# Optimization experiments

Measured on AMD Instinct MI355X. Metric: run time of the kernel, lower is better.

Reference implementation:

```python
import jax, jax.numpy as jnp
import numpy as np

HIDDEN = 4096
N_HEADS = 32
N_KV_HEADS = 8
HEAD_DIM = HIDDEN // N_HEADS  # 128
N_GROUPS = N_HEADS // N_KV_HEADS  # 4
ROPE_THETA = 10000.0
NEG_INF = -1e9


def fake_quant(x):
    """Symmetric per-tensor int8 fake quantization (quantize -> dequantize)."""
    scale = jnp.maximum(jnp.max(jnp.abs(x)) / 127.0, 1e-8)
    return jnp.clip(jnp.round(x / scale), -127.0, 127.0) * scale


def q_linear(x, W):
    # torch Linear: y = x @ W.T ; both operands fake-quantized (dequant-inline GEMM)
    return jnp.einsum('bsh,oh->bso', fake_quant(x), fake_quant(W))


def rope_cos_sin(position_ids, head_dim, dtype):
    inv_freq = 1.0 / (ROPE_THETA ** (jnp.arange(0, head_dim, 2, dtype=jnp.float32) / head_dim))
    freqs = position_ids.astype(jnp.float32)[..., None] * inv_freq  # [b, s, hd/2]
    emb = jnp.concatenate([freqs, freqs], axis=-1)                   # [b, s, hd]
    return jnp.cos(emb).astype(dtype), jnp.sin(emb).astype(dtype)


def rotate_half(x):
    x1, x2 = jnp.split(x, 2, axis=-1)
    return jnp.concatenate([-x2, x1], axis=-1)


def setup_inputs() -> dict:
    key = jax.random.key(0)
    ks = jax.random.split(key, 6)
    b, s = 2, 1024
    hidden_states = jax.random.normal(ks[0], (b, s, HIDDEN), dtype=jnp.float32)
    # additive causal mask [b, 1, q, kv]
    causal = jnp.where(jnp.tril(jnp.ones((s, s), dtype=bool)), 0.0, NEG_INF).astype(jnp.float32)
    attention_mask = jnp.broadcast_to(causal[None, None], (b, 1, s, s))
    position_ids = jnp.broadcast_to(jnp.arange(s, dtype=jnp.int64)[None, :], (b, s))
    winit = 1.0 / np.sqrt(HIDDEN)
    Wq = jax.random.normal(ks[1], (HIDDEN, HIDDEN), dtype=jnp.float32) * winit
    Wk = jax.random.normal(ks[2], (N_KV_HEADS * HEAD_DIM, HIDDEN), dtype=jnp.float32) * winit
    Wv = jax.random.normal(ks[3], (N_KV_HEADS * HEAD_DIM, HIDDEN), dtype=jnp.float32) * winit
    Wo = jax.random.normal(ks[4], (HIDDEN, HIDDEN), dtype=jnp.float32) * winit
    return {"hidden_states": hidden_states, "attention_mask": attention_mask,
            "position_ids": position_ids, "Wq": Wq, "Wk": Wk, "Wv": Wv, "Wo": Wo}


def reference(hidden_states, attention_mask, position_ids, Wq, Wk, Wv, Wo):
    b, s, _ = hidden_states.shape
    dtype = hidden_states.dtype

    # quantized QKV projections
    q = q_linear(hidden_states, Wq).reshape(b, s, N_HEADS, HEAD_DIM).transpose(0, 2, 1, 3)
    k = q_linear(hidden_states, Wk).reshape(b, s, N_KV_HEADS, HEAD_DIM).transpose(0, 2, 1, 3)
    v = q_linear(hidden_states, Wv).reshape(b, s, N_KV_HEADS, HEAD_DIM).transpose(0, 2, 1, 3)

    # RoPE
    cos, sin = rope_cos_sin(position_ids, HEAD_DIM, dtype)  # [b, s, hd]
    cos, sin = cos[:, None], sin[:, None]                   # broadcast over heads
    q = q * cos + rotate_half(q) * sin
    k = k * cos + rotate_half(k) * sin

    # GQA: repeat kv heads
    k = jnp.repeat(k, N_GROUPS, axis=1)  # [b, H, s, hd]
    v = jnp.repeat(v, N_GROUPS, axis=1)

    # quantized QK^T (per-tensor fake quant on both operands)
    attn = jnp.einsum('bhqd,bhkd->bhqk', fake_quant(q), fake_quant(k)) / jnp.sqrt(
        jnp.asarray(HEAD_DIM, dtype=jnp.float32)).astype(dtype)
    attn = attn + attention_mask
    attn = jax.nn.softmax(attn.astype(jnp.float32), axis=-1).astype(dtype)
    # attention_dropout = 0.0 (inference)

    # quantized AV matmul
    out = jnp.einsum('bhqk,bhkd->bhqd', fake_quant(attn), fake_quant(v))
    out = out.transpose(0, 2, 1, 3).reshape(b, s, HIDDEN)
    out = q_linear(out, Wo)
    return out
```

## Files before the change

### kernel.cpp

```cpp
#include <hip/hip_runtime.h>
#include <math.h>

#define B_ 2
#define S_ 1024
#define HID 4096
#define NH 32
#define NKV 8
#define HD 128
#define LOG2E 1.44269504088896340736f

typedef short s16x8 __attribute__((ext_vector_type(8)));
typedef float f32x4 __attribute__((ext_vector_type(4)));
typedef unsigned short u16;
typedef u16 u16x4 __attribute__((ext_vector_type(4)));

__device__ __forceinline__ f32x4 mfma16(s16x8 a, s16x8 b, f32x4 c) {
  return __builtin_amdgcn_mfma_f32_16x16x32_bf16(a, b, c, 0, 0, 0);
}
__device__ __forceinline__ u16 f2bf(float f) {
  union { float f; unsigned u; } v; v.f = f;
  return (u16)(v.u >> 16);
}
__device__ __forceinline__ float get_scale(const unsigned* sc, int slot) {
  return fmaxf(__uint_as_float(sc[slot]) / 127.0f, 1e-8f);
}
__device__ __forceinline__ void gload16(const void* g, void* l) {
  __builtin_amdgcn_global_load_lds(
      (const __attribute__((address_space(1))) unsigned*)g,
      (__attribute__((address_space(3))) unsigned*)l, 16, 0, 0);
}
__device__ __forceinline__ void atomic_absmax(unsigned* out, float m, int lane) {
  #pragma unroll
  for (int o = 32; o >= 1; o >>= 1) m = fmaxf(m, __shfl_xor(m, o));
  if (lane == 0) atomicMax(out, __float_as_uint(m));
}

#define SB_() __builtin_amdgcn_sched_barrier(0)
#define PBAR() do { SB_(); __builtin_amdgcn_s_barrier(); SB_(); } while (0)
#define VM6() do { SB_(); asm volatile("s_waitcnt vmcnt(6)" ::: "memory"); } while (0)
#define VM0() do { SB_(); asm volatile("s_waitcnt vmcnt(0)" ::: "memory"); } while (0)

__global__ void absmax5_k(const float4* __restrict__ p0, const float4* __restrict__ p1,
                          const float4* __restrict__ p2, const float4* __restrict__ p3,
                          const float4* __restrict__ p4, unsigned* __restrict__ sc) {
  int r = blockIdx.y;
  const float4* x; int n4;
  if (r == 0)      { x = p0; n4 = B_ * S_ * HID / 4; }
  else if (r == 1) { x = p1; n4 = HID * HID / 4; }
  else if (r == 2) { x = p2; n4 = NKV * HD * HID / 4; }
  else if (r == 3) { x = p3; n4 = NKV * HD * HID / 4; }
  else             { x = p4; n4 = HID * HID / 4; }
  float m = 0.f;
  int stride = gridDim.x * blockDim.x;
  for (int i = blockIdx.x * blockDim.x + threadIdx.x; i < n4; i += stride) {
    float4 v = x[i];
    m = fmaxf(m, fmaxf(fmaxf(fabsf(v.x), fabsf(v.y)), fmaxf(fabsf(v.z), fabsf(v.w))));
  }
  atomic_absmax(sc + r, m, threadIdx.x & 63);
}

__global__ void quant5_k(const float4* __restrict__ p0, const float4* __restrict__ p1,
                         const float4* __restrict__ p2, const float4* __restrict__ p3,
                         const float4* __restrict__ p4,
                         u16x4* __restrict__ y0, u16x4* __restrict__ y1,
                         u16x4* __restrict__ y2, u16x4* __restrict__ y3,
                         u16x4* __restrict__ y4, const unsigned* __restrict__ sc) {
  int r = blockIdx.y;
  const float4* x; u16x4* y; int n4;
  if (r == 0)      { x = p0; y = y0; n4 = B_ * S_ * HID / 4; }
  else if (r == 1) { x = p1; y = y1; n4 = HID * HID / 4; }
  else if (r == 2) { x = p2; y = y2; n4 = NKV * HD * HID / 4; }
  else if (r == 3) { x = p3; y = y3; n4 = NKV * HD * HID / 4; }
  else             { x = p4; y = y4; n4 = HID * HID / 4; }
  float s = get_scale(sc, r);
  int stride = gridDim.x * blockDim.x;
  for (int i = blockIdx.x * blockDim.x + threadIdx.x; i < n4; i += stride) {
    float4 v = x[i];
    u16x4 o;
    o[0] = f2bf(fminf(fmaxf(rintf(v.x / s), -127.f), 127.f));
    o[1] = f2bf(fminf(fmaxf(rintf(v.y / s), -127.f), 127.f));
    o[2] = f2bf(fminf(fmaxf(rintf(v.z / s), -127.f), 127.f));
    o[3] = f2bf(fminf(fmaxf(rintf(v.w / s), -127.f), 127.f));
    y[i] = o;
  }
}

__global__ void quant_k(const float4* __restrict__ x, u16x4* __restrict__ y, int n4,
                        const unsigned* __restrict__ sc, int slot) {
  float s = get_scale(sc, slot);
  int stride = gridDim.x * blockDim.x;
  for (int i = blockIdx.x * blockDim.x + threadIdx.x; i < n4; i += stride) {
    float4 v = x[i];
    u16x4 o;
    o[0] = f2bf(fminf(fmaxf(rintf(v.x / s), -127.f), 127.f));
    o[1] = f2bf(fminf(fmaxf(rintf(v.y / s), -127.f), 127.f));
    o[2] = f2bf(fminf(fmaxf(rintf(v.z / s), -127.f), 127.f));
    o[3] = f2bf(fminf(fmaxf(rintf(v.w / s), -127.f), 127.f));
    y[i] = o;
  }
}

__global__ void add_k(const float4* __restrict__ p0, const float4* __restrict__ p1,
                      float4* __restrict__ out, int n4) {
  int stride = gridDim.x * blockDim.x;
  for (int i = blockIdx.x * blockDim.x + threadIdx.x; i < n4; i += stride) {
    float4 a = p0[i], b = p1[i];
    out[i] = make_float4(a.x + b.x, a.y + b.y, a.z + b.z, a.w + b.w);
  }
}

__device__ __forceinline__ void rdA(const u16* slot, int wm, int lr, int lg,
                                    s16x8 af[4][2]) {
  #pragma unroll
  for (int mi = 0; mi < 4; ++mi) {
    int row = wm * 64 + mi * 16 + lr;
    const char* base = (const char*)slot + row * 128;
    int sw = (row & 7) << 4;
    #pragma unroll
    for (int ks = 0; ks < 2; ++ks)
      af[mi][ks] = *(const s16x8*)(base + ((ks * 64 + lg * 16) ^ sw));
  }
}
__device__ __forceinline__ void rdB(const u16* slot, int wn, int lr, int lg,
                                    s16x8 bf[2][2]) {
  #pragma unroll
  for (int ni = 0; ni < 2; ++ni) {
    int row = wn * 32 + ni * 16 + lr;
    const char* base = (const char*)slot + row * 128;
    int sw = (row & 7) << 4;
    #pragma unroll
    for (int ks = 0; ks < 2; ++ks)
      bf[ni][ks] = *(const s16x8*)(base + ((ks * 64 + lg * 16) ^ sw));
  }
}
template <int PM, int PN>
__device__ __forceinline__ void mfma_phase(f32x4 (&acc)[2][2][4][2],
                                           const s16x8 (&af)[4][2],
                                           const s16x8 (&bf)[2][2]) {
  __builtin_amdgcn_s_setprio(1);
  #pragma unroll
  for (int mi = 0; mi < 4; ++mi)
    #pragma unroll
    for (int ni = 0; ni < 2; ++ni)
      #pragma unroll
      for (int ks = 0; ks < 2; ++ks)
        acc[PM][PN][mi][ni] = mfma16(af[mi][ks], bf[ni][ks], acc[PM][PN][mi][ni]);
  __builtin_amdgcn_s_setprio(0);
}

__device__ void gemm256(const u16* __restrict__ A, const u16* __restrict__ Bm,
                        float* __restrict__ C, int Ncols, int m0, int n0,
                        int k0, int nkt, float scale, unsigned* omax, u16* S) {
  const int tid = threadIdx.x;
  const int wave = tid >> 6, lane = tid & 63;
  const int lr = lane & 15, lg = lane >> 4;
  const int wm = wave >> 2, wn = wave & 3;
  u16* SA00 = S;          u16* SA01 = S + 8192;
  u16* SB00 = S + 16384;  u16* SB01 = S + 24576;
  u16* SA10 = S + 32768;  u16* SA11 = S + 40960;
  u16* SB10 = S + 49152;  u16* SB11 = S + 57344;
  const int r0 = tid >> 3;
  const int ce = (((tid & 7) * 16) ^ ((r0 & 7) << 4)) >> 1;
  const u16* pa0 = A + (size_t)(m0 + r0) * HID + k0 + ce;
  const u16* pa1 = pa0 + (size_t)128 * HID;
  const u16* pb0 = Bm + (size_t)(n0 + r0) * HID + k0 + ce;
  const u16* pb1 = pb0 + (size_t)128 * HID;
  const int wdst = wave * 512;
  f32x4 acc[2][2][4][2] = {};
  s16x8 af[4][2], bf[2][2];

  auto STG = [&](const u16* p, u16* slot, int tcol) {
    const u16* g = p + tcol * 64;
    gload16(g, slot + wdst);
    gload16(g + (size_t)64 * HID, slot + 4096 + wdst);
  };

  STG(pa0, SA00, 0); STG(pb0, SB00, 0); STG(pa1, SA01, 0); STG(pb1, SB01, 0);
  STG(pa0, SA10, 1); STG(pb1, SB11, 1); STG(pa1, SA11, 1);
  VM6(); PBAR();

  #pragma unroll 1
  for (int t = 0; t < nkt; t += 2) {
    const bool g2 = t + 2 < nkt, g3 = t + 3 < nkt;
    rdA(SA00, wm, lr, lg, af); rdB(SB00, wn, lr, lg, bf);
    STG(pb0, SB10, t + 1);
    PBAR(); mfma_phase<0, 0>(acc, af, bf); PBAR();
    rdB(SB01, wn, lr, lg, bf);
    if (g2) STG(pa0, SA00, t + 2);
    PBAR(); mfma_phase<0, 1>(acc, af, bf); PBAR();
    rdA(SA01, wm, lr, lg, af);
    if (g2) STG(pb1, SB01, t + 2);
    PBAR(); mfma_phase<1, 1>(acc, af, bf); PBAR();
    rdB(SB00, wn, lr, lg, bf);
    if (g2) STG(pa1, SA01, t + 2);
    PBAR(); mfma_phase<1, 0>(acc, af, bf);
    if (g2) { VM6(); } else { VM0(); }
    PBAR();
    rdA(SA10, wm, lr, lg, af); rdB(SB10, wn, lr, lg, bf);
    if (g2) STG(pb0, SB00, t + 2);
    PBAR(); mfma_phase<0, 0>(acc, af, bf); PBAR();
    rdB(SB11, wn, lr, lg, bf);
    if (g3) STG(pa0, SA10, t + 3);
    PBAR(); mfma_phase<0, 1>(acc, af, bf); PBAR();
    rdA(SA11, wm, lr, lg, af);
    if (g3) STG(pb1, SB11, t + 3);
    PBAR(); mfma_phase<1, 1>(acc, af, bf); PBAR();
    rdB(SB10, wn, lr, lg, bf);
    if (g3) STG(pa1, SA11, t + 3);
    PBAR(); mfma_phase<1, 0>(acc, af, bf); VM6(); PBAR();
  }

  float gm = 0.f;
  #pragma unroll
  for (int mh = 0; mh < 2; ++mh)
    #pragma unroll
    for (int nh = 0; nh < 2; ++nh)
      #pragma unroll
      for (int mi = 0; mi < 4; ++mi)
        #pragma unroll
        for (int ni = 0; ni < 2; ++ni) {
          size_t rbase = (size_t)(m0 + mh * 128 + wm * 64 + mi * 16 + lg * 4);
          int cb = n0 + nh * 128 + wn * 32 + ni * 16 + lr;
          #pragma unroll
          for (int r = 0; r < 4; ++r) {
            float v = acc[mh][nh][mi][ni][r] * scale;
            gm = fmaxf(gm, fabsf(v));
            C[(rbase + r) * (size_t)Ncols + cb] = v;
          }
        }
  if (omax) atomic_absmax(omax, gm, lane);
}

__global__ __launch_bounds__(512, 1) void gemm_qkv8(
    const u16* __restrict__ Xq, const u16* __restrict__ Wqb,
    const u16* __restrict__ Wkb, const u16* __restrict__ Wvb,
    float* __restrict__ qf, float* __restrict__ kf, float* __restrict__ vf,
    const unsigned* __restrict__ sc, unsigned* __restrict__ vmax) {
  extern __shared__ __align__(16) u16 S[];
  int raw = blockIdx.x;
  int wg = (raw & 7) * 24 + (raw >> 3);
  int bx = wg & 7, by = wg >> 3;
  const u16* Bm; float* C; int Ncols, n0, sslot; unsigned* om = nullptr;
  if (by < 16)      { Bm = Wqb; C = qf; Ncols = HID;      n0 = by * 256;        sslot = 1; }
  else if (by < 20) { Bm = Wkb; C = kf; Ncols = NKV * HD; n0 = (by - 16) * 256; sslot = 2; }
  else              { Bm = Wvb; C = vf; Ncols = NKV * HD; n0 = (by - 20) * 256; sslot = 3; om = vmax; }
  float scale = get_scale(sc, 0) * get_scale(sc, sslot);
  gemm256(Xq, Bm, C, Ncols, bx * 256, n0, 0, 64, scale, om, S);
}

__global__ __launch_bounds__(512, 1) void gemm_o8(
    const u16* __restrict__ A, const u16* __restrict__ Bm,
    float* __restrict__ P0, float* __restrict__ P1,
    const unsigned* __restrict__ sc) {
  extern __shared__ __align__(16) u16 S[];
  int raw = blockIdx.x;
  int wg = (raw & 7) * 32 + (raw >> 3);
  int tile = wg >> 1, half = wg & 1;
  int by = tile & 15, bx = tile >> 4;
  float scale = get_scale(sc, 8) * get_scale(sc, 4);
  gemm256(A, Bm, half ? P1 : P0, HID, bx * 256, by * 256, half * 2048, 32,
          scale, nullptr, S);
}

__global__ void rope_tab_k(float2* __restrict__ tab) {
  int i = blockIdx.x * 256 + threadIdx.x;
  int pos = i >> 6, d = i & 63;
  float inv = exp2f((float)d * (-13.287712379549449f / 64.0f));
  float ang = (float)pos * inv;
  tab[i] = make_float2(cosf(ang), sinf(ang));
}

__global__ void rope2_k(float* __restrict__ qf, float* __restrict__ kf,
                        unsigned* __restrict__ sc, const float2* __restrict__ tab) {
  int reg = blockIdx.y;
  float* q = reg ? kf : qf;
  int nheads = reg ? NKV : NH;
  unsigned* om = sc + (reg ? 6 : 5);
  int total = B_ * S_ * nheads * 64;
  int stride = gridDim.x * blockDim.x;
  float m = 0.f;
  for (int i = blockIdx.x * blockDim.x + threadIdx.x; i < total; i += stride) {
    int d = i & 63;
    int h = (i >> 6) % nheads;
    int bs = i / (64 * nheads);
    int pos = bs & (S_ - 1);
    float2 cs = tab[(pos << 6) + d];
    size_t base = ((size_t)bs * nheads + h) * HD + d;
    float x1 = q[base], x2 = q[base + 64];
    float o1 = x1 * cs.x - x2 * cs.y;
    float o2 = x2 * cs.x + x1 * cs.y;
    q[base] = o1; q[base + 64] = o2;
    m = fmaxf(m, fmaxf(fabsf(o1), fabsf(o2)));
  }
  atomic_absmax(om, m, threadIdx.x & 63);
}

__global__ void quantqk_k(const float4* __restrict__ qf, const float4* __restrict__ kf,
                          u16x4* __restrict__ qq, u16x4* __restrict__ kq,
                          const unsigned* __restrict__ sc) {
  int reg = blockIdx.y;
  const float4* x = reg ? kf : qf;
  u16x4* y = reg ? kq : qq;
  int n4 = reg ? (B_ * S_ * NKV * HD / 4) : (B_ * S_ * HID / 4);
  float s = get_scale(sc, reg ? 6 : 5);
  int stride = gridDim.x * blockDim.x;
  for (int i = blockIdx.x * blockDim.x + threadIdx.x; i < n4; i += stride) {
    float4 v = x[i];
    u16x4 o;
    o[0] = f2bf(fminf(fmaxf(rintf(v.x / s), -127.f), 127.f));
    o[1] = f2bf(fminf(fmaxf(rintf(v.y / s), -127.f), 127.f));
    o[2] = f2bf(fminf(fmaxf(rintf(v.z / s), -127.f), 127.f));
    o[3] = f2bf(fminf(fmaxf(rintf(v.w / s), -127.f), 127.f));
    y[i] = o;
  }
}

__global__ __launch_bounds__(256) void vquant_t_k(const float* __restrict__ vf,
                                                  unsigned* __restrict__ vtw,
                                                  const unsigned* __restrict__ sc) {
  __shared__ u16 Ls[64 * 132];
  float s = get_scale(sc, 7);
  int st = blockIdx.x & 15, kvh = (blockIdx.x >> 4) & 7, b = blockIdx.x >> 7;
  int s0 = st * 64;
  #pragma unroll
  for (int i = 0; i < 8; ++i) {
    int o = i * 256 + threadIdx.x;
    int sr = o >> 5, c4 = o & 31;
    float4 v = *(const float4*)(vf + ((size_t)(b * S_ + s0 + sr)) * (NKV * HD) +
                                kvh * HD + c4 * 4);
    u16x4 w;
    w[0] = f2bf(fminf(fmaxf(rintf(v.x / s), -127.f), 127.f));
    w[1] = f2bf(fminf(fmaxf(rintf(v.y / s), -127.f), 127.f));
    w[2] = f2bf(fminf(fmaxf(rintf(v.z / s), -127.f), 127.f));
    w[3] = f2bf(fminf(fmaxf(rintf(v.w / s), -127.f), 127.f));
    *(u16x4*)(Ls + sr * 132 + c4 * 4) = w;
  }
  __syncthreads();
  #pragma unroll
  for (int i = 0; i < 16; ++i) {
    int o = i * 256 + threadIdx.x;
    int d = o >> 5, sj = o & 31;
    unsigned lo = Ls[(sj * 2) * 132 + d], hi = Ls[(sj * 2 + 1) * 132 + d];
    vtw[(((size_t)(b * NKV + kvh) * HD + d) << 9) + st * 32 + sj] = lo | (hi << 16);
  }
}

__global__ __launch_bounds__(512) void attn_k(
    const u16* __restrict__ Q, const u16* __restrict__ Kq, const u16* __restrict__ Vt,
    float* __restrict__ O, const unsigned* __restrict__ sc, unsigned* __restrict__ omax) {
  __shared__ __align__(16) u16 Ks[2][64 * 128];
  __shared__ __align__(16) u16 Vs[2][128 * 64];
  __shared__ __align__(16) u16 Ps[128 * 64];
  const int tid = threadIdx.x;
  const int wave = tid >> 6, lane = tid & 63;
  const int lr = lane & 15, lg = lane >> 4;
  const int raw = blockIdx.x;
  const int xcd = raw & 7, j = raw >> 3;
  const int grp = xcd + 8 * (j >> 4);
  const int within = j & 15;
  const int b = grp >> 3, kvh = grp & 7;
  const int h = kvh * 4 + (within >> 2);
  const int qp = within & 3;
  const float sq = get_scale(sc, 5), sk = get_scale(sc, 6), sv = get_scale(sc, 7);
  const float c2 = sq * sk * 0.08838834764831845f * LOG2E;
  const float M0 = 32.0f;
  const int k_rin = lane >> 4;
  const int k_cb0 = (lane & 15) * 16;
  const int v_rin = lane >> 3;
  const int v_cb = ((lane & 7) * 16) ^ ((v_rin & 7) << 4);
  float gmax = 0.f;

  auto stageK = [&](int buf, int kt) {
    #pragma unroll
    for (int i = 0; i < 2; ++i) {
      int ch = wave * 2 + i;
      int row = ch * 4 + k_rin;
      int cb = k_cb0 ^ ((row & 7) << 4);
      gload16(Kq + (size_t)(b * S_ + kt * 64 + row) * (NKV * HD) + kvh * HD + (cb >> 1),
              Ks[buf] + ch * 512);
    }
  };
  auto stageV = [&](int buf, int kt) {
    #pragma unroll
    for (int i = 0; i < 2; ++i) {
      int ch = wave * 2 + i;
      int vrow = ch * 8 + v_rin;
      gload16(Vt + ((size_t)(b * NKV + kvh) * HD + vrow) * S_ + kt * 64 + (v_cb >> 1),
              Vs[buf] + ch * 512);
    }
  };

  for (int pi = 0; pi < 2; ++pi) {
    const int qt = pi ? 7 - qp : qp;
    const int q0 = qt * 128;
    const int nkt = 2 * (qt + 1);
    const int qwmin = q0 + wave * 16;
    s16x8 aq[4];
    {
      const u16* qp_ = Q + (size_t)(b * S_ + q0 + wave * 16 + lr) * HID + h * HD + lg * 8;
      #pragma unroll
      for (int ks = 0; ks < 4; ++ks) aq[ks] = *(const s16x8*)(qp_ + ks * 32);
    }
    float ll[4] = {0.f, 0.f, 0.f, 0.f};

    stageK(0, 0);
    __syncthreads();
    for (int kt = 0; kt < nkt; ++kt) {
      const int p = kt & 1;
      if (kt < nkt - 1) stageK(p ^ 1, kt + 1);
      f32x4 sacc[4] = {};
      __builtin_amdgcn_s_setprio(1);
      #pragma unroll
      for (int ks = 0; ks < 4; ++ks)
        #pragma unroll
        for (int n = 0; n < 4; ++n) {
          int row = n * 16 + lr;
          s16x8 bk = *(const s16x8*)((const char*)Ks[p] + row * 256 +
                                     ((ks * 64 + lg * 16) ^ ((row & 7) << 4)));
          sacc[n] = mfma16(aq[ks], bk, sacc[n]);
        }
      __builtin_amdgcn_s_setprio(0);
      if (kt * 64 + 63 <= qwmin) {
        #pragma unroll
        for (int r = 0; r < 4; ++r)
          #pragma unroll
          for (int n = 0; n < 4; ++n)
            ll[r] += exp2f(fmaf(sacc[n][r], c2, -M0));
      } else {
        #pragma unroll
        for (int r = 0; r < 4; ++r) {
          int qg = qwmin + lg * 4 + r;
          #pragma unroll
          for (int n = 0; n < 4; ++n) {
            int kg = kt * 64 + n * 16 + lr;
            float e = exp2f(fmaf(sacc[n][r], c2, -M0));
            ll[r] += (kg <= qg) ? e : 0.f;
          }
        }
      }
      __syncthreads();
    }
    float bias[4];
    #pragma unroll
    for (int r = 0; r < 4; ++r) {
      float l = ll[r];
      #pragma unroll
      for (int o = 8; o >= 1; o >>= 1) l += __shfl_xor(l, o);
      bias[r] = 6.9886846867721655f - __log2f(l) - M0;
    }

    f32x4 oacc[8] = {};
    stageK(0, 0); stageV(0, 0);
    __syncthreads();
    for (int kt = 0; kt < nkt; ++kt) {
      const int p = kt & 1;
      if (kt < nkt - 1) { stageK(p ^ 1, kt + 1); stageV(p ^ 1, kt + 1); }
      f32x4 sacc[4] = {};
      __builtin_amdgcn_s_setprio(1);
      #pragma unroll
      for (int ks = 0; ks < 4; ++ks)
        #pragma unroll
        for (int n = 0; n < 4; ++n) {
          int row = n * 16 + lr;
          s16x8 bk = *(const s16x8*)((const char*)Ks[p] + row * 256 +
                                     ((ks * 64 + lg * 16) ^ ((row & 7) << 4)));
          sacc[n] = mfma16(aq[ks], bk, sacc[n]);
        }
      __builtin_amdgcn_s_setprio(0);
      if (kt * 64 + 63 <= qwmin) {
        #pragma unroll
        for (int r = 0; r < 4; ++r) {
          int prow = wave * 16 + lg * 4 + r;
          #pragma unroll
          for (int n = 0; n < 4; ++n) {
            float p127 = rintf(exp2f(fmaf(sacc[n][r], c2, bias[r])));
            int col = n * 16 + lr;
            *(u16*)((char*)Ps + prow * 128 + ((col * 2) ^ ((prow & 7) << 4))) = f2bf(p127);
          }
        }
      } else {
        #pragma unroll
        for (int r = 0; r < 4; ++r) {
          int prow = wave * 16 + lg * 4 + r;
          int qg = qwmin + lg * 4 + r;
          #pragma unroll
          for (int n = 0; n < 4; ++n) {
            int kg = kt * 64 + n * 16 + lr;
            float a = fmaf(sacc[n][r], c2, bias[r]);
            float p127 = (kg <= qg) ? rintf(exp2f(a)) : 0.f;
            int col = n * 16 + lr;
            *(u16*)((char*)Ps + prow * 128 + ((col * 2) ^ ((prow & 7) << 4))) = f2bf(p127);
          }
        }
      }
      __builtin_amdgcn_s_setprio(1);
      #pragma unroll
      for (int ks = 0; ks < 2; ++ks) {
        int prow = wave * 16 + lr;
        s16x8 ap = *(const s16x8*)((const char*)Ps + prow * 128 +
                                   ((ks * 64 + lg * 16) ^ ((prow & 7) << 4)));
        #pragma unroll
        for (int n = 0; n < 8; ++n) {
          int vrow = n * 16 + lr;
          s16x8 bv = *(const s16x8*)((const char*)Vs[p] + vrow * 128 +
                                     ((ks * 64 + lg * 16) ^ ((vrow & 7) << 4)));
          oacc[n] = mfma16(ap, bv, oacc[n]);
        }
      }
      __builtin_amdgcn_s_setprio(0);
      __syncthreads();
    }
    const float pvs = sv * (1.0f / 127.0f);
    #pragma unroll
    for (int n = 0; n < 8; ++n)
      #pragma unroll
      for (int r = 0; r < 4; ++r) {
        float v = oacc[n][r] * pvs;
        gmax = fmaxf(gmax, fabsf(v));
        O[(size_t)(b * S_ + q0 + wave * 16 + lg * 4 + r) * HID + h * HD + n * 16 + lr] = v;
      }
  }
  atomic_absmax(omax, gmax, lane);
}

extern "C" void kernel_launch(void* const* d_in, const int* in_sizes, int n_in,
                              void* d_out, int out_size, void* d_ws, size_t ws_size,
                              hipStream_t stream) {
  const float* hs = (const float*)d_in[0];
  const float* Wq = (const float*)d_in[3];
  const float* Wk = (const float*)d_in[4];
  const float* Wv = (const float*)d_in[5];
  const float* Wo = (const float*)d_in[6];
  float* out = (float*)d_out;
  char* ws = (char*)d_ws;

  unsigned* sc = (unsigned*)ws;
  size_t off = 256;
  u16* Xq = (u16*)(ws + off); off += (size_t)B_ * S_ * HID * 2;
  size_t wqb_off = off;
  u16* Wqb = (u16*)(ws + off); off += (size_t)HID * HID * 2;
  u16* Wkb = (u16*)(ws + off); off += (size_t)NKV * HD * HID * 2;
  u16* Wvb = (u16*)(ws + off); off += (size_t)NKV * HD * HID * 2;
  u16* Wob = (u16*)(ws + off); off += (size_t)HID * HID * 2;
  size_t qf_off = off;
  float* qf = (float*)(ws + off); off += (size_t)B_ * S_ * HID * 4;
  size_t kf_off = off;
  float* kf = (float*)(ws + off); off += (size_t)B_ * S_ * NKV * HD * 4;
  float* vf = (float*)(ws + off); off += (size_t)B_ * S_ * NKV * HD * 4;
  u16* qq = (u16*)(ws + off); off += (size_t)B_ * S_ * HID * 2;
  u16* kq = (u16*)(ws + off); off += (size_t)B_ * S_ * NKV * HD * 2;
  u16* vt = (u16*)(ws + off); off += (size_t)B_ * S_ * NKV * HD * 2;
  float2* tab = (float2*)(ws + off); off += (size_t)S_ * 64 * 8;
  float* attnf = (float*)(ws + qf_off);
  u16* attnq = (u16*)(ws + wqb_off);
  float* P0 = (float*)(ws + qf_off);
  float* P1 = (float*)(ws + kf_off);

  hipFuncSetAttribute((const void*)gemm_qkv8,
                      hipFuncAttributeMaxDynamicSharedMemorySize, 131072);
  hipFuncSetAttribute((const void*)gemm_o8,
                      hipFuncAttributeMaxDynamicSharedMemorySize, 131072);

  hipMemsetAsync(sc, 0, 64, stream);

  dim3 blk(256);
  absmax5_k<<<dim3(416, 5), blk, 0, stream>>>(
      (const float4*)hs, (const float4*)Wq, (const float4*)Wk,
      (const float4*)Wv, (const float4*)Wo, sc);
  quant5_k<<<dim3(416, 5), blk, 0, stream>>>(
      (const float4*)hs, (const float4*)Wq, (const float4*)Wk,
      (const float4*)Wv, (const float4*)Wo,
      (u16x4*)Xq, (u16x4*)Wqb, (u16x4*)Wkb, (u16x4*)Wvb, (u16x4*)Wob, sc);
  rope_tab_k<<<256, blk, 0, stream>>>(tab);

  gemm_qkv8<<<192, 512, 131072, stream>>>(Xq, Wqb, Wkb, Wvb, qf, kf, vf, sc, sc + 7);

  rope2_k<<<dim3(512, 2), blk, 0, stream>>>(qf, kf, sc, tab);
  quantqk_k<<<dim3(512, 2), blk, 0, stream>>>((const float4*)qf, (const float4*)kf,
                                              (u16x4*)qq, (u16x4*)kq, sc);
  vquant_t_k<<<256, blk, 0, stream>>>(vf, (unsigned*)vt, sc);

  attn_k<<<256, 512, 0, stream>>>(qq, kq, vt, attnf, sc, sc + 8);

  quant_k<<<2048, blk, 0, stream>>>((const float4*)attnf, (u16x4*)attnq,
                                    B_ * S_ * HID / 4, sc, 8);
  gemm_o8<<<256, 512, 131072, stream>>>(attnq, Wob, P0, P1, sc);
  add_k<<<2048, blk, 0, stream>>>((const float4*)P0, (const float4*)P1,
                                  (float4*)out, B_ * S_ * HID / 4);
}
```

Measured before the change: 558.0 us.

## Switch projection GEMMs from bf16 to int8 MFMA with int32 accumulation

The quantize kernels now pack the fake-quantized integer values as int8 bytes instead of bf16, and the QKV and output projection GEMMs use the i32 16x16x64 int8 MFMA. Each K tile now covers 128 elements in the same LDS footprint, which halves the number of K iterations, the operand bytes moved, and the quantized-weight traffic. Results stay exact because the values are integers in [-127,127] and the int32 accumulators cannot overflow at K=4096. The risk is that the LDS swizzle and tile indexing had to be reworked for byte elements, and the hidden loop body has to agree with the new slot offsets.

```diff
diff --git a/kernel.cpp b/kernel.cpp
--- a/kernel.cpp
+++ b/kernel.cpp
@@ -11,11 +11,16 @@
 
 typedef short s16x8 __attribute__((ext_vector_type(8)));
 typedef float f32x4 __attribute__((ext_vector_type(4)));
+typedef int i32x4 __attribute__((ext_vector_type(4)));
 typedef unsigned short u16;
 typedef u16 u16x4 __attribute__((ext_vector_type(4)));
+typedef signed char s8;
 
 __device__ __forceinline__ f32x4 mfma16(s16x8 a, s16x8 b, f32x4 c) {
   return __builtin_amdgcn_mfma_f32_16x16x32_bf16(a, b, c, 0, 0, 0);
+}
+__device__ __forceinline__ i32x4 mfma_i8(i32x4 a, i32x4 b, i32x4 c) {
+  return __builtin_amdgcn_mfma_i32_16x16x64_i8(a, b, c, 0, 0, 0);
 }
 __device__ __forceinline__ u16 f2bf(float f) {
   union { float f; unsigned u; } v; v.f = f;
@@ -23,6 +28,13 @@
 }
 __device__ __forceinline__ float get_scale(const unsigned* sc, int slot) {
   return fmaxf(__uint_as_float(sc[slot]) / 127.0f, 1e-8f);
+}
+__device__ __forceinline__ int q127(float x, float s) {
+  return (int)fminf(fmaxf(rintf(x / s), -127.f), 127.f);
+}
+__device__ __forceinline__ unsigned pack4(float4 v, float s) {
+  return (q127(v.x, s) & 255) | ((q127(v.y, s) & 255) << 8) |
+         ((q127(v.z, s) & 255) << 16) | ((q127(v.w, s) & 255) << 24);
 }
 __device__ __forceinline__ void gload16(const void* g, void* l) {
   __builtin_amdgcn_global_load_lds(
@@ -62,11 +74,11 @@
 __global__ void quant5_k(const float4* __restrict__ p0, const float4* __restrict__ p1,
                          const float4* __restrict__ p2, const float4* __restrict__ p3,
                          const float4* __restrict__ p4,
-                         u16x4* __restrict__ y0, u16x4* __restrict__ y1,
-                         u16x4* __restrict__ y2, u16x4* __restrict__ y3,
-                         u16x4* __restrict__ y4, const unsigned* __restrict__ sc) {
+                         unsigned* __restrict__ y0, unsigned* __restrict__ y1,
+                         unsigned* __restrict__ y2, unsigned* __restrict__ y3,
+                         unsigned* __restrict__ y4, const unsigned* __restrict__ sc) {
   int r = blockIdx.y;
-  const float4* x; u16x4* y; int n4;
+  const float4* x; unsigned* y; int n4;
   if (r == 0)      { x = p0; y = y0; n4 = B_ * S_ * HID / 4; }
   else if (r == 1) { x = p1; y = y1; n4 = HID * HID / 4; }
   else if (r == 2) { x = p2; y = y2; n4 = NKV * HD * HID / 4; }
@@ -74,30 +86,16 @@
   else             { x = p4; y = y4; n4 = HID * HID / 4; }
   float s = get_scale(sc, r);
   int stride = gridDim.x * blockDim.x;
-  for (int i = blockIdx.x * blockDim.x + threadIdx.x; i < n4; i += stride) {
-    float4 v = x[i];
-    u16x4 o;
-    o[0] = f2bf(fminf(fmaxf(rintf(v.x / s), -127.f), 127.f));
-    o[1] = f2bf(fminf(fmaxf(rintf(v.y / s), -127.f), 127.f));
-    o[2] = f2bf(fminf(fmaxf(rintf(v.z / s), -127.f), 127.f));
-    o[3] = f2bf(fminf(fmaxf(rintf(v.w / s), -127.f), 127.f));
-    y[i] = o;
-  }
-}
-
-__global__ void quant_k(const float4* __restrict__ x, u16x4* __restrict__ y, int n4,
+  for (int i = blockIdx.x * blockDim.x + threadIdx.x; i < n4; i += stride)
+    y[i] = pack4(x[i], s);
+}
+
+__global__ void quant_k(const float4* __restrict__ x, unsigned* __restrict__ y, int n4,
                         const unsigned* __restrict__ sc, int slot) {
   float s = get_scale(sc, slot);
   int stride = gridDim.x * blockDim.x;
-  for (int i = blockIdx.x * blockDim.x + threadIdx.x; i < n4; i += stride) {
-    float4 v = x[i];
-    u16x4 o;
-    o[0] = f2bf(fminf(fmaxf(rintf(v.x / s), -127.f), 127.f));
-    o[1] = f2bf(fminf(fmaxf(rintf(v.y / s), -127.f), 127.f));
-    o[2] = f2bf(fminf(fmaxf(rintf(v.z / s), -127.f), 127.f));
-    o[3] = f2bf(fminf(fmaxf(rintf(v.w / s), -127.f), 127.f));
-    y[i] = o;
-  }
+  for (int i = blockIdx.x * blockDim.x + threadIdx.x; i < n4; i += stride)
+    y[i] = pack4(x[i], s);
 }
 
 __global__ void add_k(const float4* __restrict__ p0, const float4* __restrict__ p1,
@@ -109,8 +107,8 @@
   }
 }
 
-__device__ __forceinline__ void rdA(const u16* slot, int wm, int lr, int lg,
-                                    s16x8 af[4][2]) {
+__device__ __forceinline__ void rdA(const s8* slot, int wm, int lr, int lg,
+                                    i32x4 af[4][2]) {
   #pragma unroll
   for (int mi = 0; mi < 4; ++mi) {
     int row = wm * 64 + mi * 16 + lr;
@@ -118,11 +116,11 @@
     int sw = (row & 7) << 4;
     #pragma unroll
     for (int ks = 0; ks < 2; ++ks)
-      af[mi][ks] = *(const s16x8*)(base + ((ks * 64 + lg * 16) ^ sw));
-  }
-}
-__device__ __forceinline__ void rdB(const u16* slot, int wn, int lr, int lg,
-                                    s16x8 bf[2][2]) {
+      af[mi][ks] = *(const i32x4*)(base + ((ks * 64 + lg * 16) ^ sw));
+  }
+}
+__device__ __forceinline__ void rdB(const s8* slot, int wn, int lr, int lg,
+                                    i32x4 bf[2][2]) {
   #pragma unroll
   for (int ni = 0; ni < 2; ++ni) {
     int row = wn * 32 + ni * 16 + lr;
@@ -130,13 +128,13 @@
     int sw = (row & 7) << 4;
     #pragma unroll
     for (int ks = 0; ks < 2; ++ks)
-      bf[ni][ks] = *(const s16x8*)(base + ((ks * 64 + lg * 16) ^ sw));
+      bf[ni][ks] = *(const i32x4*)(base + ((ks * 64 + lg * 16) ^ sw));
   }
 }
 template <int PM, int PN>
-__device__ __forceinline__ void mfma_phase(f32x4 (&acc)[2][2][4][2],
-                                           const s16x8 (&af)[4][2],
-                                           const s16x8 (&bf)[2][2]) {
+__device__ __forceinline__ void mfma_phase(i32x4 (&acc)[2][2][4][2],
+                                           const i32x4 (&af)[4][2],
+                                           const i32x4 (&bf)[2][2]) {
   __builtin_amdgcn_s_setprio(1);
   #pragma unroll
   for (int mi = 0; mi < 4; ++mi)
@@ -144,35 +142,35 @@
     for (int ni = 0; ni < 2; ++ni)
       #pragma unroll
       for (int ks = 0; ks < 2; ++ks)
-        acc[PM][PN][mi][ni] = mfma16(af[mi][ks], bf[ni][ks], acc[PM][PN][mi][ni]);
+        acc[PM][PN][mi][ni] = mfma_i8(af[mi][ks], bf[ni][ks], acc[PM][PN][mi][ni]);
   __builtin_amdgcn_s_setprio(0);
 }
 
-__device__ void gemm256(const u16* __restrict__ A, const u16* __restrict__ Bm,
+__device__ void gemm256(const s8* __restrict__ A, const s8* __restrict__ Bm,
                         float* __restrict__ C, int Ncols, int m0, int n0,
-                        int k0, int nkt, float scale, unsigned* omax, u16* S) {
+                        int k0, int nkt, float scale, unsigned* omax, s8* S) {
   const int tid = threadIdx.x;
   const int wave = tid >> 6, lane = tid & 63;
   const int lr = lane & 15, lg = lane >> 4;
   const int wm = wave >> 2, wn = wave & 3;
-  u16* SA00 = S;          u16* SA01 = S + 8192;
-  u16* SB00 = S + 16384;  u16* SB01 = S + 24576;
-  u16* SA10 = S + 32768;  u16* SA11 = S + 40960;
-  u16* SB10 = S + 49152;  u16* SB11 = S + 57344;
+  s8* SA00 = S;          s8* SA01 = S + 16384;
+  s8* SB00 = S + 32768;  s8* SB01 = S + 49152;
+  s8* SA10 = S + 65536;  s8* SA11 = S + 81920;
+  s8* SB10 = S + 98304;  s8* SB11 = S + 114688;
   const int r0 = tid >> 3;
-  const int ce = (((tid & 7) * 16) ^ ((r0 & 7) << 4)) >> 1;
-  const u16* pa0 = A + (size_t)(m0 + r0) * HID + k0 + ce;
-  const u16* pa1 = pa0 + (size_t)128 * HID;
-  const u16* pb0 = Bm + (size_t)(n0 + r0) * HID + k0 + ce;
-  const u16* pb1 = pb0 + (size_t)128 * HID;
-  const int wdst = wave * 512;
-  f32x4 acc[2][2][4][2] = {};
-  s16x8 af[4][2], bf[2][2];
-
-  auto STG = [&](const u16* p, u16* slot, int tcol) {
-    const u16* g = p + tcol * 64;
+  const int ce = ((tid & 7) * 16) ^ ((r0 & 7) << 4);
+  const s8* pa0 = A + (size_t)(m0 + r0) * HID + k0 + ce;
+  const s8* pa1 = pa0 + (size_t)128 * HID;
+  const s8* pb0 = Bm + (size_t)(n0 + r0) * HID + k0 + ce;
+  const s8* pb1 = pb0 + (size_t)128 * HID;
+  const int wdst = wave * 1024;
+  i32x4 acc[2][2][4][2] = {};
+  i32x4 af[4][2], bf[2][2];
+
+  auto STG = [&](const s8* p, s8* slot, int tcol) {
+    const s8* g = p + tcol * 128;
     gload16(g, slot + wdst);
-    gload16(g + (size_t)64 * HID, slot + 4096 + wdst);
+    gload16(g + (size_t)64 * HID, slot + 8192 + wdst);
   };
 
   STG(pa0, SA00, 0); STG(pb0, SB00, 0); STG(pa1, SA01, 0); STG(pb1, SB01, 0);
@@ -223,7 +221,7 @@
           int cb = n0 + nh * 128 + wn * 32 + ni * 16 + lr;
           #pragma unroll
           for (int r = 0; r < 4; ++r) {
-            float v = acc[mh][nh][mi][ni][r] * scale;
+            float v = (float)acc[mh][nh][mi][ni][r] * scale;
             gm = fmaxf(gm, fabsf(v));
             C[(rbase + r) * (size_t)Ncols + cb] = v;
           }
@@ -232,33 +230,33 @@
 }
 
 __global__ __launch_bounds__(512, 1) void gemm_qkv8(
-    const u16* __restrict__ Xq, const u16* __restrict__ Wqb,
-    const u16* __restrict__ Wkb, const u16* __restrict__ Wvb,
+    const s8* __restrict__ Xq, const s8* __restrict__ Wqb,
+    const s8* __restrict__ Wkb, const s8* __restrict__ Wvb,
     float* __restrict__ qf, float* __restrict__ kf, float* __restrict__ vf,
     const unsigned* __restrict__ sc, unsigned* __restrict__ vmax) {
-  extern __shared__ __align__(16) u16 S[];
+  extern __shared__ __align__(16) s8 S[];
   int raw = blockIdx.x;
   int wg = (raw & 7) * 24 + (raw >> 3);
   int bx = wg & 7, by = wg >> 3;
-  const u16* Bm; float* C; int Ncols, n0, sslot; unsigned* om = nullptr;
+  const s8* Bm; float* C; int Ncols, n0, sslot; unsigned* om = nullptr;
   if (by < 16)      { Bm = Wqb; C = qf; Ncols = HID;      n0 = by * 256;        sslot = 1; }
   else if (by < 20) { Bm = Wkb; C = kf; Ncols = NKV * HD; n0 = (by - 16) * 256; sslot = 2; }
   else              { Bm = Wvb; C = vf; Ncols = NKV * HD; n0 = (by - 20) * 256; sslot = 3; om = vmax; }
   float scale = get_scale(sc, 0) * get_scale(sc, sslot);
-  gemm256(Xq, Bm, C, Ncols, bx * 256, n0, 0, 64, scale, om, S);
+  gemm256(Xq, Bm, C, Ncols, bx * 256, n0, 0, 32, scale, om, S);
 }
 
 __global__ __launch_bounds__(512, 1) void gemm_o8(
-    const u16* __restrict__ A, const u16* __restrict__ Bm,
+    const s8* __restrict__ A, const s8* __restrict__ Bm,
     float* __restrict__ P0, float* __restrict__ P1,
     const unsigned* __restrict__ sc) {
-  extern __shared__ __align__(16) u16 S[];
+  extern __shared__ __align__(16) s8 S[];
   int raw = blockIdx.x;
   int wg = (raw & 7) * 32 + (raw >> 3);
   int tile = wg >> 1, half = wg & 1;
   int by = tile & 15, bx = tile >> 4;
   float scale = get_scale(sc, 8) * get_scale(sc, 4);
-  gemm256(A, Bm, half ? P1 : P0, HID, bx * 256, by * 256, half * 2048, 32,
+  gemm256(A, Bm, half ? P1 : P0, HID, bx * 256, by * 256, half * 2048, 16,
           scale, nullptr, S);
 }
 
@@ -536,12 +534,12 @@
 
   unsigned* sc = (unsigned*)ws;
   size_t off = 256;
-  u16* Xq = (u16*)(ws + off); off += (size_t)B_ * S_ * HID * 2;
+  s8* Xq = (s8*)(ws + off); off += (size_t)B_ * S_ * HID;
   size_t wqb_off = off;
-  u16* Wqb = (u16*)(ws + off); off += (size_t)HID * HID * 2;
-  u16* Wkb = (u16*)(ws + off); off += (size_t)NKV * HD * HID * 2;
-  u16* Wvb = (u16*)(ws + off); off += (size_t)NKV * HD * HID * 2;
-  u16* Wob = (u16*)(ws + off); off += (size_t)HID * HID * 2;
+  s8* Wqb = (s8*)(ws + off); off += (size_t)HID * HID;
+  s8* Wkb = (s8*)(ws + off); off += (size_t)NKV * HD * HID;
+  s8* Wvb = (s8*)(ws + off); off += (size_t)NKV * HD * HID;
+  s8* Wob = (s8*)(ws + off); off += (size_t)HID * HID;
   size_t qf_off = off;
   float* qf = (float*)(ws + off); off += (size_t)B_ * S_ * HID * 4;
   size_t kf_off = off;
@@ -552,7 +550,7 @@
   u16* vt = (u16*)(ws + off); off += (size_t)B_ * S_ * NKV * HD * 2;
   float2* tab = (float2*)(ws + off); off += (size_t)S_ * 64 * 8;
   float* attnf = (float*)(ws + qf_off);
-  u16* attnq = (u16*)(ws + wqb_off);
+  s8* attnq = (s8*)(ws + wqb_off);
   float* P0 = (float*)(ws + qf_off);
   float* P1 = (float*)(ws + kf_off);
 
@@ -570,7 +568,8 @@
   quant5_k<<<dim3(416, 5), blk, 0, stream>>>(
       (const float4*)hs, (const float4*)Wq, (const float4*)Wk,
       (const float4*)Wv, (const float4*)Wo,
-      (u16x4*)Xq, (u16x4*)Wqb, (u16x4*)Wkb, (u16x4*)Wvb, (u16x4*)Wob, sc);
+      (unsigned*)Xq, (unsigned*)Wqb, (unsigned*)Wkb, (unsigned*)Wvb,
+      (unsigned*)Wob, sc);
   rope_tab_k<<<256, blk, 0, stream>>>(tab);
 
   gemm_qkv8<<<192, 512, 131072, stream>>>(Xq, Wqb, Wkb, Wvb, qf, kf, vf, sc, sc + 7);
@@ -582,7 +581,7 @@
 
   attn_k<<<256, 512, 0, stream>>>(qq, kq, vt, attnf, sc, sc + 8);
 
-  quant_k<<<2048, blk, 0, stream>>>((const float4*)attnf, (u16x4*)attnq,
+  quant_k<<<2048, blk, 0, stream>>>((const float4*)attnf, (unsigned*)attnq,
                                     B_ * S_ * HID / 4, sc, 8);
   gemm_o8<<<256, 512, 131072, stream>>>(attnq, Wob, P0, P1, sc);
   add_k<<<2048, blk, 0, stream>>>((const float4*)P0, (const float4*)P1,
```

After: 468.6 us. -16.0%, faster.
